# Performance work log

Measured on AMD Instinct MI355X. Metric: run time of the kernel, lower is better.

The kernel has to match this reference:

```python
import jax, jax.numpy as jnp
import numpy as np

EPSILON = 1e-8
MATCH_THRESHOLD = 0.5
MEANINGFUL_RADIUS = 0.05


def setup_inputs() -> dict:
    key = jax.random.key(0)
    ks = jax.random.split(key, 8)
    B, T, H, D, N = 4, 4096, 2048, 256, 8192
    K = H // 4
    s = lambda k, shape, fan_in: jax.random.normal(k, shape, jnp.float32) * (fan_in ** -0.5)
    return {
        "hidden": jax.random.normal(ks[0], (B, T, H), jnp.float32),
        "beliefs": jax.random.normal(ks[1], (N, D), jnp.float32),
        "active_mask": jax.random.bernoulli(ks[2], 0.9, (N,)),
        "W_obs": s(ks[3], (D, H), H),
        "W_g1": s(ks[4], (K, H), H),
        "b_g1": jnp.zeros((K,), jnp.float32),
        "W_g2": s(ks[5], (1, K), K),
        "b_g2": jnp.full((1,), -2.0, jnp.float32),  # nn.init.constant_(bias, -2.0)
        "W_p1": s(ks[6], (K, H), H),
        "b_p1": jnp.zeros((K,), jnp.float32),
        "W_p2": s(ks[7], (1, K), K),
        "b_p2": jnp.zeros((1,), jnp.float32),
    }


def reference(hidden, beliefs, active_mask, W_obs, W_g1, b_g1, W_g2, b_g2, W_p1, b_p1, W_p2, b_p2):
    # --- projections over [B, T, H] ---
    obs = jnp.einsum('bth,dh->btd', hidden, W_obs)                       # [B,T,D]
    g_h = jax.nn.relu(jnp.einsum('bth,kh->btk', hidden, W_g1) + b_g1)
    gate = jax.nn.sigmoid(jnp.einsum('btk,ok->bto', g_h, W_g2) + b_g2)   # [B,T,1]
    p_h = jax.nn.relu(jnp.einsum('bth,kh->btk', hidden, W_p1) + b_p1)
    prec = jax.nn.softplus(jnp.einsum('btk,ok->bto', p_h, W_p2) + b_p2)  # [B,T,1]

    obs_mean = obs.mean(axis=0)            # [T,D]
    prec_mean = (gate * prec).mean(axis=0)  # [T,1]

    # F.normalize(x, dim=-1, eps) == x / max(||x||, eps)
    obs_angles = obs_mean / jnp.maximum(
        jnp.linalg.norm(obs_mean, axis=-1, keepdims=True), EPSILON)
    obs_beliefs = obs_angles * prec_mean    # [T,D], radius = gated precision

    # --- match against active belief slots (fully vectorized, no per-token loop) ---
    obs_r = jnp.linalg.norm(obs_beliefs, axis=-1)                       # [T]
    obs_ang = obs_beliefs / jnp.maximum(obs_r, EPSILON)[:, None]
    bel_r = jnp.maximum(jnp.linalg.norm(beliefs, axis=-1), EPSILON)     # [N]
    bel_ang = beliefs / bel_r[:, None]

    sims = obs_ang @ bel_ang.T              # [T,N] cosine similarities
    neg = jnp.finfo(sims.dtype).min
    masked = jnp.where(active_mask[None, :], sims, neg)
    any_active = jnp.any(active_mask)
    best_sims = jnp.where(any_active, masked.max(axis=-1), 0.0)         # [T]
    best_idx = jnp.where(any_active, jnp.argmax(masked, axis=-1), -1)   # [T]

    meaningful = obs_r > MEANINGFUL_RADIUS
    matched = meaningful & (best_sims > MATCH_THRESHOLD)
    matched_slot = jnp.where(matched, best_idx, -1)                     # -1 == new slot
    match_sim = jnp.where(matched, best_sims, 0.0)

    # vectorized stand-in for list[WriteCandidate]:
    # belief vectors, per-token match similarity, matched slot id, validity mask
    return obs_beliefs, match_sim, matched_slot, meaningful
```

## Files before the change

kernel.cpp:

```cpp
#include <hip/hip_runtime.h>

constexpr int B = 4, T = 4096, H = 2048, D = 256, KK = 512, N = 8192;
constexpr int BT = B * T;
constexpr int NALL = 1280;
constexpr int CAP = 1536;

typedef short bf16x8 __attribute__((ext_vector_type(8)));
typedef float f32x4  __attribute__((ext_vector_type(4)));

__device__ __forceinline__ unsigned short f2bf(float f) {
    unsigned u = __float_as_uint(f);
    return (unsigned short)((u + 0x7fffu + ((u >> 16) & 1u)) >> 16);
}
__device__ __forceinline__ float bf2f(unsigned short h) {
    return __uint_as_float((unsigned)h << 16);
}
__device__ __forceinline__ void async16(const void* g, void* l) {
    __builtin_amdgcn_global_load_lds(
        (const __attribute__((address_space(1))) unsigned int*)g,
        (__attribute__((address_space(3))) unsigned int*)l, 16, 0, 0);
}
__device__ __forceinline__ unsigned long long enc_sim(float s, int idx) {
    unsigned bits = __float_as_uint(s);
    unsigned e32 = (bits & 0x80000000u) ? ~bits : (bits | 0x80000000u);
    return ((unsigned long long)e32 << 32) | (unsigned)(~(unsigned)idx);
}

constexpr size_t WS_HB   = 0;
constexpr size_t WS_WB   = WS_HB   + (size_t)BT * H * 2;
constexpr size_t WS_BELB = WS_WB   + (size_t)NALL * H * 2;
constexpr size_t WS_OAB  = WS_BELB + (size_t)N * D * 2;
constexpr size_t WS_B1C  = WS_OAB  + (size_t)T * D * 2;
constexpr size_t WS_W2C  = WS_B1C  + 4096;
constexpr size_t WS_FAC  = WS_W2C  + 4096;
constexpr size_t WS_OBSR = WS_FAC  + 16384;
constexpr size_t WS_FLAG = WS_OBSR + 16384;
constexpr size_t WS_OBS  = WS_FLAG + (size_t)CAP * 4;
constexpr size_t WS_YG   = WS_OBS  + (size_t)T * D * 4;
constexpr size_t WS_YP   = WS_YG   + (size_t)BT * 4;
constexpr size_t WS_ENC  = WS_YP   + (size_t)BT * 4;
constexpr size_t WS_CNT  = WS_ENC  + (size_t)T * 8;
constexpr size_t WS_ACTV = WS_CNT  + 256;
constexpr size_t WS_META = WS_ACTV + (size_t)N * 4;
constexpr size_t WS_NEEDF = WS_META + 256;
constexpr size_t WS_ZEROSZ = WS_ACTV - WS_OBS;

constexpr int    WTC    = 1280;
constexpr size_t F_WT   = 0;
constexpr size_t F_BEL  = F_WT   + (size_t)H * WTC * 4;
constexpr size_t F_OBS  = F_BEL  + (size_t)N * D * 4;
constexpr size_t F_YG   = F_OBS  + (size_t)T * D * 4;
constexpr size_t F_YP   = F_YG   + (size_t)BT * 4;
constexpr size_t F_OBSR = F_YP   + (size_t)BT * 4;
constexpr size_t F_ENC  = F_OBSR + (size_t)T * 4;
constexpr size_t F_ACT  = F_ENC  + (size_t)T * 8;
constexpr size_t F_META = F_ACT  + (size_t)N * 4;
constexpr size_t F_NEED = F_META + 256;

__global__ void mask_kernel(const unsigned char* raw, int* active, int* meta) {
    __shared__ int s_f32bad, s_nz_nonaligned;
    if (threadIdx.x == 0) { s_f32bad = 0; s_nz_nonaligned = 0; }
    __syncthreads();
    const float* rf = (const float*)raw;
    const int*   ri = (const int*)raw;
    for (int i = threadIdx.x; i < N; i += blockDim.x) {
        unsigned char b = raw[i];
        if ((i & 3) && b) atomicOr(&s_nz_nonaligned, 1);
    }
    for (int e = threadIdx.x; e < N / 4; e += blockDim.x) {
        float f = rf[e]; if (!(f == 0.0f || f == 1.0f)) atomicOr(&s_f32bad, 1);
    }
    __syncthreads();
    int layout;
    if (!s_f32bad)            layout = 2;
    else if (s_nz_nonaligned) layout = 1;
    else                      layout = 0;
    for (int n = threadIdx.x; n < N; n += blockDim.x) {
        int a;
        if (layout == 2)      a = (rf[n] != 0.0f);
        else if (layout == 1) a = (raw[n] != 0);
        else                  a = (ri[n] != 0);
        active[n] = a;
    }
    if (threadIdx.x == 0) meta[0] = layout;
}

__global__ void outw_kernel(const unsigned long long* enc, const float* obs_r_ws,
                            float* out1, float* out2) {
    int t = blockIdx.x * 256 + threadIdx.x;
    if (t >= T) return;
    unsigned long long ev = enc[t];
    float best; int idx;
    if (ev == 0ULL) { best = -3.4e38f; idx = -1; }
    else {
        unsigned int e32 = (unsigned int)(ev >> 32);
        unsigned int bits = (e32 & 0x80000000u) ? (e32 & 0x7FFFFFFFu) : ~e32;
        best = __uint_as_float(bits);
        idx = (int)~((unsigned int)(ev & 0xFFFFFFFFu));
    }
    bool meaningful = obs_r_ws[t] > 0.05f;
    bool matched = meaningful && (best > 0.5f);
    out1[t] = matched ? best : 0.0f;
    out2[t] = matched ? (float)idx : -1.0f;
}

__global__ void conv_hidden(const float* hidden, unsigned short* hb) {
    int e = blockIdx.x * 256 + threadIdx.x;
    int row = e >> 8, c8 = (e & 255) * 8;
    const float* src = hidden + (size_t)row * H + c8;
    float4 v0 = *(const float4*)src;
    float4 v1 = *(const float4*)(src + 4);
    uint4 o;
    o.x = f2bf(v0.x) | ((unsigned)f2bf(v0.y) << 16);
    o.y = f2bf(v0.z) | ((unsigned)f2bf(v0.w) << 16);
    o.z = f2bf(v1.x) | ((unsigned)f2bf(v1.y) << 16);
    o.w = f2bf(v1.z) | ((unsigned)f2bf(v1.w) << 16);
    *(uint4*)(hb + (size_t)row * H + c8) = o;
}

__global__ void conv_wb(const float* Wg1, const float* Wp1, const float* Wobs,
                        unsigned short* wb) {
    int e = blockIdx.x * 256 + threadIdx.x;
    int row = e >> 8, c8 = (e & 255) * 8;
    const float* src = (row < 512) ? &Wg1[(size_t)row * H]
                     : (row < 1024) ? &Wp1[(size_t)(row - 512) * H]
                                    : &Wobs[(size_t)(row - 1024) * H];
    float4 v0 = *(const float4*)(src + c8);
    float4 v1 = *(const float4*)(src + c8 + 4);
    uint4 o;
    o.x = f2bf(v0.x) | ((unsigned)f2bf(v0.y) << 16);
    o.y = f2bf(v0.z) | ((unsigned)f2bf(v0.w) << 16);
    o.z = f2bf(v1.x) | ((unsigned)f2bf(v1.y) << 16);
    o.w = f2bf(v1.z) | ((unsigned)f2bf(v1.w) << 16);
    *(uint4*)(wb + (size_t)row * H + c8) = o;
}

__global__ void conv_vec(const float* b_g1, const float* b_p1, const float* W_g2,
                         const float* W_p2, float* b1c, float* w2c) {
    int c = threadIdx.x;
    if (c < 512) { b1c[c] = b_g1[c];       w2c[c] = W_g2[c]; }
    else         { b1c[c] = b_p1[c - 512]; w2c[c] = W_p2[c - 512]; }
}

__global__ void belprep_bf(const float* beliefs, unsigned short* belb) {
    int wave = (blockIdx.x * blockDim.x + threadIdx.x) >> 6;
    int lane = threadIdx.x & 63;
    if (wave >= N) return;
    float4 v = ((const float4*)(beliefs + (size_t)wave * D))[lane];
    float ss = v.x * v.x + v.y * v.y + v.z * v.z + v.w * v.w;
    for (int m = 1; m < 64; m <<= 1) ss += __shfl_xor(ss, m, 64);
    float inv = 1.0f / fmaxf(sqrtf(ss), 1e-8f);
    uint2 o;
    o.x = f2bf(v.x * inv) | ((unsigned)f2bf(v.y * inv) << 16);
    o.y = f2bf(v.z * inv) | ((unsigned)f2bf(v.w * inv) << 16);
    *(uint2*)(belb + (size_t)wave * D + lane * 4) = o;
}

__global__ __launch_bounds__(256) void big_gemm(const unsigned short* Ab, const unsigned short* Bb,
                                                const float* b1c, const float* w2c,
                                                float* yg, float* yp, float* obs_buf) {
    __shared__ unsigned short As[128 * 32];
    __shared__ unsigned short Bs[128 * 32];
    __shared__ float b1s[128], w2s[128];
    int tid = threadIdx.x;
    int mb = blockIdx.x, nb = blockIdx.y;
    int m0 = mb * 128, n0 = nb * 128;
    bool is_mlp = (nb < 8);
    if (is_mlp && tid < 128) { b1s[tid] = b1c[n0 + tid]; w2s[tid] = w2c[n0 + tid]; }
    int wave = tid >> 6, lane = tid & 63;
    int wr = wave >> 1, wc = wave & 1;
    int quad = lane >> 4, mrow = lane & 15;
    f32x4 acc[4][4] = {};
    const unsigned short* gA = Ab + (size_t)(m0 + (tid >> 2)) * H + (tid & 3) * 8;
    const unsigned short* gB = Bb + (size_t)(n0 + (tid >> 2)) * H + (tid & 3) * 8;
    char* lA = (char*)As + wave * 1024;
    char* lB = (char*)Bs + wave * 1024;
    for (int k0 = 0; k0 < H; k0 += 32) {
        async16(gA + k0, lA);
        async16(gA + (size_t)64 * H + k0, lA + 4096);
        async16(gB + k0, lB);
        async16(gB + (size_t)64 * H + k0, lB + 4096);
        __syncthreads();
        bf16x8 a[4], b[4];
        for (int i = 0; i < 4; i++) a[i] = *(const bf16x8*)&As[(wr * 64 + i * 16 + mrow) * 32 + quad * 8];
        for (int j = 0; j < 4; j++) b[j] = *(const bf16x8*)&Bs[(wc * 64 + j * 16 + mrow) * 32 + quad * 8];
        for (int i = 0; i < 4; i++)
            for (int j = 0; j < 4; j++)
                acc[i][j] = __builtin_amdgcn_mfma_f32_16x16x32_bf16(a[i], b[j], acc[i][j], 0, 0, 0);
        __syncthreads();
    }
    if (is_mlp) {
        float* y = (nb < 4) ? yg : yp;
        for (int i = 0; i < 4; i++) {
            int row_g = m0 + wr * 64 + i * 16 + quad * 4;
            for (int r = 0; r < 4; r++) {
                float s = 0.0f;
                for (int j = 0; j < 4; j++) {
                    int cl = wc * 64 + j * 16 + mrow;
                    float z = acc[i][j][r] + b1s[cl];
                    z = fmaxf(z, 0.0f);
                    s += z * w2s[cl];
                }
                s += __shfl_xor(s, 1); s += __shfl_xor(s, 2);
                s += __shfl_xor(s, 4); s += __shfl_xor(s, 8);
                if (mrow == 0) atomicAdd(&y[row_g + r], s);
            }
        }
    } else {
        for (int i = 0; i < 4; i++)
            for (int r = 0; r < 4; r++) {
                int row_g = m0 + wr * 64 + i * 16 + quad * 4 + r;
                int t = row_g & (T - 1);
                for (int j = 0; j < 4; j++) {
                    int d = n0 - 1024 + wc * 64 + j * 16 + mrow;
                    atomicAdd(&obs_buf[(size_t)t * D + d], acc[i][j][r] * 0.25f);
                }
            }
    }
}

__global__ void finalize_fast(const float* yg, const float* yp, const float* obs_buf,
                              const float* b_g2, const float* b_p2,
                              float* out0, float* out3, float* obs_r_ws, float* fac,
                              unsigned short* oab, int* flaglist, int* flagcnt,
                              float* yg_mut, float* yp_mut) {
    int t = blockIdx.x * 4 + (threadIdx.x >> 6);
    int lane = threadIdx.x & 63;
    if (t >= T) return;
    float bg2 = b_g2[0], bp2 = b_p2[0];
    float pm = 0.0f;
    for (int b = 0; b < B; ++b) {
        float g = yg[b * T + t] + bg2;
        float p = yp[b * T + t] + bp2;
        float gate = 1.0f / (1.0f + expf(-g));
        float prec = (p > 20.0f) ? p : log1pf(expf(p));
        pm += gate * prec;
    }
    pm *= 0.25f;
    float4 v = ((const float4*)(obs_buf + (size_t)t * D))[lane];
    float ss = v.x * v.x + v.y * v.y + v.z * v.z + v.w * v.w;
    for (int m = 1; m < 64; m <<= 1) ss += __shfl_xor(ss, m, 64);
    float norm = sqrtf(ss);
    float na = fmaxf(norm, 1e-8f);
    float f = norm / na;
    float inv = 1.0f / na;
    float ax = v.x * inv, ay = v.y * inv, az = v.z * inv, aw = v.w * inv;
    float4 ob; ob.x = ax * pm; ob.y = ay * pm; ob.z = az * pm; ob.w = aw * pm;
    ((float4*)(out0 + (size_t)t * D))[lane] = ob;
    uint2 oa;
    oa.x = f2bf(ax) | ((unsigned)f2bf(ay) << 16);
    oa.y = f2bf(az) | ((unsigned)f2bf(aw) << 16);
    *(uint2*)(oab + (size_t)t * D + lane * 4) = oa;
    if (lane == 0) {
        float obs_r = pm * f;
        obs_r_ws[t] = obs_r;
        fac[t] = f;
        out3[t] = (obs_r > 0.05f) ? 1.0f : 0.0f;
        if (fabsf(obs_r - 0.05f) < 1.2e-3f) {
            int idx = atomicAdd(flagcnt, 1);
            if (idx < CAP) {
                flaglist[idx] = t;
                for (int b = 0; b < B; ++b) { yg_mut[b * T + t] = 0.0f; yp_mut[b * T + t] = 0.0f; }
            }
        }
    }
}

__global__ __launch_bounds__(256) void refine_mfma(const float* hidden,
        const float* W_g1, const float* W_p1, const float* b1c, const float* w2c,
        const int* flaglist, const int* flagcnt, float* yg, float* yp) {
    int nrows = min(*flagcnt, CAP) * 4;
    int m0 = blockIdx.x * 64;
    if (m0 >= nrows) return;
    int nb = blockIdx.y;
    int n0 = nb * 128;
    __shared__ unsigned short Ahi[64 * 32], Alo[64 * 32];
    __shared__ unsigned short Bhi[128 * 32], Blo[128 * 32];
    __shared__ int rowg_s[64];
    __shared__ float b1s[128], w2s[128];
    int tid = threadIdx.x;
    if (tid < 64) {
        int fr = m0 + tid;
        int rg = -1;
        if (fr < nrows) { int tok = flaglist[fr >> 2]; rg = (fr & 3) * T + tok; }
        rowg_s[tid] = rg;
    } else if (tid >= 128) {
        int c = tid - 128;
        b1s[c] = b1c[n0 + c]; w2s[c] = w2c[n0 + c];
    }
    __syncthreads();
    const float* Wbase = (n0 < 512) ? W_g1 : W_p1;
    int wofs = n0 & 511;
    int arow = tid >> 2, kseg = (tid & 3) * 8;
    int argr = rowg_s[arow]; if (argr < 0) argr = 0;
    const float* aptr = hidden + (size_t)argr * H + kseg;
    const float* bptr0 = Wbase + (size_t)(wofs + arow) * H + kseg;
    const float* bptr1 = Wbase + (size_t)(wofs + arow + 64) * H + kseg;
    int wave = tid >> 6, lane = tid & 63;
    int quad = lane >> 4, mrow = lane & 15;
    f32x4 acc[4][2] = {};
    for (int k0 = 0; k0 < H; k0 += 32) {
        float xs[8];
        {
            float4 v0 = *(const float4*)(aptr + k0);
            float4 v1 = *(const float4*)(aptr + k0 + 4);
            xs[0]=v0.x; xs[1]=v0.y; xs[2]=v0.z; xs[3]=v0.w;
            xs[4]=v1.x; xs[5]=v1.y; xs[6]=v1.z; xs[7]=v1.w;
            unsigned short hi[8], lo[8];
            for (int q = 0; q < 8; q++) {
                hi[q] = f2bf(xs[q]);
                lo[q] = f2bf(xs[q] - bf2f(hi[q]));
            }
            uint4 ph, pl;
            ph.x = hi[0]|((unsigned)hi[1]<<16); ph.y = hi[2]|((unsigned)hi[3]<<16);
            ph.z = hi[4]|((unsigned)hi[5]<<16); ph.w = hi[6]|((unsigned)hi[7]<<16);
            pl.x = lo[0]|((unsigned)lo[1]<<16); pl.y = lo[2]|((unsigned)lo[3]<<16);
            pl.z = lo[4]|((unsigned)lo[5]<<16); pl.w = lo[6]|((unsigned)lo[7]<<16);
            *(uint4*)&Ahi[arow * 32 + kseg] = ph;
            *(uint4*)&Alo[arow * 32 + kseg] = pl;
        }
        for (int half = 0; half < 2; half++) {
            const float* bp = half ? bptr1 : bptr0;
            float4 v0 = *(const float4*)(bp + k0);
            float4 v1 = *(const float4*)(bp + k0 + 4);
            xs[0]=v0.x; xs[1]=v0.y; xs[2]=v0.z; xs[3]=v0.w;
            xs[4]=v1.x; xs[5]=v1.y; xs[6]=v1.z; xs[7]=v1.w;
            unsigned short hi[8], lo[8];
            for (int q = 0; q < 8; q++) {
                hi[q] = f2bf(xs[q]);
                lo[q] = f2bf(xs[q] - bf2f(hi[q]));
            }
            uint4 ph, pl;
            ph.x = hi[0]|((unsigned)hi[1]<<16); ph.y = hi[2]|((unsigned)hi[3]<<16);
            ph.z = hi[4]|((unsigned)hi[5]<<16); ph.w = hi[6]|((unsigned)hi[7]<<16);
            pl.x = lo[0]|((unsigned)lo[1]<<16); pl.y = lo[2]|((unsigned)lo[3]<<16);
            pl.z = lo[4]|((unsigned)lo[5]<<16); pl.w = lo[6]|((unsigned)lo[7]<<16);
            *(uint4*)&Bhi[(arow + half * 64) * 32 + kseg] = ph;
            *(uint4*)&Blo[(arow + half * 64) * 32 + kseg] = pl;
        }
        __syncthreads();
        bf16x8 ah[4], al[4], bh[2], bl[2];
        for (int i = 0; i < 4; i++) {
            ah[i] = *(const bf16x8*)&Ahi[(i * 16 + mrow) * 32 + quad * 8];
            al[i] = *(const bf16x8*)&Alo[(i * 16 + mrow) * 32 + quad * 8];
        }
        for (int j = 0; j < 2; j++) {
            bh[j] = *(const bf16x8*)&Bhi[(wave * 32 + j * 16 + mrow) * 32 + quad * 8];
            bl[j] = *(const bf16x8*)&Blo[(wave * 32 + j * 16 + mrow) * 32 + quad * 8];
        }
        for (int i = 0; i < 4; i++)
            for (int j = 0; j < 2; j++) {
                acc[i][j] = __builtin_amdgcn_mfma_f32_16x16x32_bf16(al[i], bh[j], acc[i][j], 0, 0, 0);
                acc[i][j] = __builtin_amdgcn_mfma_f32_16x16x32_bf16(ah[i], bl[j], acc[i][j], 0, 0, 0);
                acc[i][j] = __builtin_amdgcn_mfma_f32_16x16x32_bf16(ah[i], bh[j], acc[i][j], 0, 0, 0);
            }
        __syncthreads();
    }
    float* y = (nb < 4) ? yg : yp;
    for (int i = 0; i < 4; i++)
        for (int r = 0; r < 4; r++) {
            int row_l = i * 16 + quad * 4 + r;
            float s = 0.0f;
            for (int j = 0; j < 2; j++) {
                int cl = wave * 32 + j * 16 + mrow;
                float z = fmaxf(acc[i][j][r] + b1s[cl], 0.0f);
                s += z * w2s[cl];
            }
            s += __shfl_xor(s, 1); s += __shfl_xor(s, 2);
            s += __shfl_xor(s, 4); s += __shfl_xor(s, 8);
            if (mrow == 0) {
                int rg = rowg_s[row_l];
                if (rg >= 0) atomicAdd(&y[rg], s);
            }
        }
}

__global__ void refine_pm(const float* yg, const float* yp, const float* b_g2, const float* b_p2,
                          const int* flagcnt, const int* flaglist, const float* fac,
                          float* obs_r_ws, float* out3) {
    int nflag = min(*flagcnt, CAP);
    int idx = blockIdx.x * 64 + threadIdx.x;
    if (idx >= nflag) return;
    int t = flaglist[idx];
    float bg2 = b_g2[0], bp2 = b_p2[0];
    float pm = 0.0f;
    for (int b = 0; b < B; ++b) {
        float g = yg[b * T + t] + bg2;
        float p = yp[b * T + t] + bp2;
        float gate = 1.0f / (1.0f + expf(-g));
        float prec = (p > 20.0f) ? p : log1pf(expf(p));
        pm += gate * prec;
    }
    pm *= 0.25f;
    float obs_r = pm * fac[t];
    obs_r_ws[t] = obs_r;
    out3[t] = (obs_r > 0.05f) ? 1.0f : 0.0f;
}

__global__ __launch_bounds__(256) void sims_mfma(const unsigned short* oab, const unsigned short* belb,
                                                 const int* active, unsigned long long* enc) {
    __shared__ unsigned short As[128 * 32];
    __shared__ unsigned short Bs[128 * 32];
    __shared__ int acts[128];
    int tid = threadIdx.x;
    int mb = blockIdx.x, nb = blockIdx.y;
    int m0 = mb * 128, n0 = nb * 128;
    if (tid < 128) acts[tid] = active[n0 + tid];
    int wave = tid >> 6, lane = tid & 63;
    int wr = wave >> 1, wc = wave & 1;
    int quad = lane >> 4, mrow = lane & 15;
    f32x4 acc[4][4] = {};
    const unsigned short* gA = oab + (size_t)(m0 + (tid >> 2)) * D + (tid & 3) * 8;
    const unsigned short* gB = belb + (size_t)(n0 + (tid >> 2)) * D + (tid & 3) * 8;
    char* lA = (char*)As + wave * 1024;
    char* lB = (char*)Bs + wave * 1024;
    for (int k0 = 0; k0 < D; k0 += 32) {
        async16(gA + k0, lA);
        async16(gA + (size_t)64 * D + k0, lA + 4096);
        async16(gB + k0, lB);
        async16(gB + (size_t)64 * D + k0, lB + 4096);
        __syncthreads();
        bf16x8 a[4], b[4];
        for (int i = 0; i < 4; i++) a[i] = *(const bf16x8*)&As[(wr * 64 + i * 16 + mrow) * 32 + quad * 8];
        for (int j = 0; j < 4; j++) b[j] = *(const bf16x8*)&Bs[(wc * 64 + j * 16 + mrow) * 32 + quad * 8];
        for (int i = 0; i < 4; i++)
            for (int j = 0; j < 4; j++)
                acc[i][j] = __builtin_amdgcn_mfma_f32_16x16x32_bf16(a[i], b[j], acc[i][j], 0, 0, 0);
        __syncthreads();
    }
    for (int i = 0; i < 4; i++)
        for (int r = 0; r < 4; r++) {
            int row_g = m0 + wr * 64 + i * 16 + quad * 4 + r;
            unsigned long long best = 0ULL;
            for (int j = 0; j < 4; j++) {
                int cl = wc * 64 + j * 16 + mrow;
                if (acts[cl]) {
                    unsigned long long ev = enc_sim(acc[i][j][r], n0 + cl);
                    if (ev > best) best = ev;
                }
            }
            best = max(best, __shfl_xor(best, 1));
            best = max(best, __shfl_xor(best, 2));
            best = max(best, __shfl_xor(best, 4));
            best = max(best, __shfl_xor(best, 8));
            if (mrow == 0 && best) atomicMax(&enc[row_g], best);
        }
}

__global__ void wt_kernel(const float* Wg1, const float* Wp1, const float* Wobs, float* WT) {
    __shared__ float tile[32][33];
    int hb = blockIdx.x * 32, cb = blockIdx.y * 32;
    int x = threadIdx.x & 31, y = threadIdx.x >> 5;
    for (int i = 0; i < 32; i += 8) {
        int c = cb + y + i;
        const float* src = (c < 512) ? &Wg1[(size_t)c * H]
                         : (c < 1024) ? &Wp1[(size_t)(c - 512) * H]
                                      : &Wobs[(size_t)(c - 1024) * H];
        tile[y + i][x] = src[hb + x];
    }
    __syncthreads();
    for (int i = 0; i < 32; i += 8)
        WT[(size_t)(hb + y + i) * WTC + cb + x] = tile[x][y + i];
}

__global__ void belprep_kernel(const float* beliefs, float* bel_ang) {
    int wave = (blockIdx.x * blockDim.x + threadIdx.x) >> 6;
    int lane = threadIdx.x & 63;
    if (wave >= N) return;
    float4 v = ((const float4*)(beliefs + (size_t)wave * D))[lane];
    float ss = v.x * v.x + v.y * v.y + v.z * v.z + v.w * v.w;
    for (int m = 1; m < 64; m <<= 1) ss += __shfl_xor(ss, m, 64);
    float inv = 1.0f / fmaxf(sqrtf(ss), 1e-8f);
    float4 o; o.x = v.x * inv; o.y = v.y * inv; o.z = v.z * inv; o.w = v.w * inv;
    ((float4*)(bel_ang + (size_t)wave * D))[lane] = o;
}

__global__ __launch_bounds__(256) void gemm_obs_kernel(const float* hidden, const float* WT,
                                                       float* obs_mean) {
    __shared__ float As[32][33];
    __shared__ float Ws[32][260];
    int t0 = blockIdx.x * 32;
    int tx = threadIdx.x & 63, ty = threadIdx.x >> 6;
    float acc[8][4] = {};
    for (int h0 = 0; h0 < H; h0 += 32) {
        for (int q = 0; q < 4; ++q) {
            int e = threadIdx.x + q * 256;
            int r = e >> 5, kk = e & 31;
            float s = 0.0f;
            for (int b = 0; b < B; ++b) s += hidden[((size_t)b * T + t0 + r) * H + h0 + kk];
            As[kk][r] = s;
        }
        for (int q = 0; q < 8; ++q) {
            int e4 = threadIdx.x + q * 256;
            int kk = e4 >> 6, c4 = (e4 & 63) * 4;
            *(float4*)&Ws[kk][c4] = *(const float4*)&WT[(size_t)(h0 + kk) * WTC + 1024 + c4];
        }
        __syncthreads();
        for (int kk = 0; kk < 32; ++kk) {
            float a[8], w[4];
            for (int i = 0; i < 8; i++) a[i] = As[kk][ty * 8 + i];
            for (int j = 0; j < 4; j++) w[j] = Ws[kk][tx + 64 * j];
            for (int i = 0; i < 8; i++)
                for (int j = 0; j < 4; j++) acc[i][j] += a[i] * w[j];
        }
        __syncthreads();
    }
    for (int i = 0; i < 8; i++)
        for (int j = 0; j < 4; j++)
            obs_mean[(size_t)(t0 + ty * 8 + i) * D + tx + 64 * j] = acc[i][j] * 0.25f;
}

__global__ __launch_bounds__(512, 4) void gemm_mlp_kernel(
        const float* hidden, const float* WT,
        const float* b1g, const float* b1p, const float* w2g, const float* w2p,
        const float* b2g, const float* b2p, float* yg, float* yp) {
    __shared__ float As[16][65];
    __shared__ float Ws[16][516];
    int R = blockIdx.x * 64;
    int path = blockIdx.y;
    int cbase = path * 512;
    int tx = threadIdx.x & 63, ty = threadIdx.x >> 6;
    float acc[8][8] = {};
    for (int h0 = 0; h0 < H; h0 += 16) {
        {   int r = threadIdx.x >> 3, k2 = (threadIdx.x & 7) * 2;
            float2 v = *(const float2*)&hidden[(size_t)(R + r) * H + h0 + k2];
            As[k2][r] = v.x; As[k2 + 1][r] = v.y; }
        for (int q = 0; q < 4; ++q) {
            int e4 = threadIdx.x + q * 512;
            int kk = e4 >> 7, c4 = (e4 & 127) * 4;
            *(float4*)&Ws[kk][c4] = *(const float4*)&WT[(size_t)(h0 + kk) * WTC + cbase + c4];
        }
        __syncthreads();
        for (int kk = 0; kk < 16; ++kk) {
            float a[8], w[8];
            for (int i = 0; i < 8; i++) a[i] = As[kk][ty * 8 + i];
            for (int j = 0; j < 8; j++) w[j] = Ws[kk][tx + 64 * j];
            for (int i = 0; i < 8; i++)
                for (int j = 0; j < 8; j++) acc[i][j] += a[i] * w[j];
        }
        __syncthreads();
    }
    const float* b1 = path ? b1p : b1g;
    const float* w2 = path ? w2p : w2g;
    float b2 = path ? b2p[0] : b2g[0];
    float part[8];
    for (int i = 0; i < 8; i++) {
        float s = 0.0f;
        for (int j = 0; j < 8; j++) {
            int c = tx + 64 * j;
            float z = fmaxf(acc[i][j] + b1[c], 0.0f);
            s += z * w2[c];
        }
        part[i] = s;
    }
    for (int m = 1; m < 64; m <<= 1)
        for (int i = 0; i < 8; i++) part[i] += __shfl_xor(part[i], m, 64);
    if (tx == 0) {
        float* dst = path ? yp : yg;
        for (int i = 0; i < 8; i++) dst[R + ty * 8 + i] = part[i] + b2;
    }
}

__global__ void finalize_kernel(const float* yg, const float* yp, float* obs,
                                float* out0, float* out3, float* obs_r_ws,
                                unsigned long long* enc) {
    int t = blockIdx.x * 4 + (threadIdx.x >> 6);
    int lane = threadIdx.x & 63;
    if (t >= T) return;
    float pm = 0.0f;
    for (int b = 0; b < B; ++b) {
        float g = yg[b * T + t], p = yp[b * T + t];
        float gate = 1.0f / (1.0f + expf(-g));
        float prec = (p > 15.0f) ? p : log1pf(expf(p));
        pm += gate * prec;
    }
    pm *= (1.0f / B);
    float4 v = ((const float4*)(obs + (size_t)t * D))[lane];
    float ss = v.x * v.x + v.y * v.y + v.z * v.z + v.w * v.w;
    for (int m = 1; m < 64; m <<= 1) ss += __shfl_xor(ss, m, 64);
    float norm = sqrtf(ss);
    float na = fmaxf(norm, 1e-8f);
    float4 ob;
    ob.x = v.x / na * pm; ob.y = v.y / na * pm;
    ob.z = v.z / na * pm; ob.w = v.w / na * pm;
    float obs_r = pm * (norm / na);
    ((float4*)(out0 + (size_t)t * D))[lane] = ob;
    float ra = fmaxf(obs_r, 1e-8f);
    float4 oa;
    oa.x = ob.x / ra; oa.y = ob.y / ra; oa.z = ob.z / ra; oa.w = ob.w / ra;
    ((float4*)(obs + (size_t)t * D))[lane] = oa;
    if (lane == 0) {
        out3[t] = (obs_r > 0.05f) ? 1.0f : 0.0f;
        obs_r_ws[t] = obs_r;
        enc[t] = 0ULL;
    }
}

__global__ __launch_bounds__(256) void sims_kernel(const float* obs_ang, const float* bel_ang,
                                                   const int* active, unsigned long long* enc) {
    __shared__ float Aos[64][68];
    __shared__ float Bbs[64][68];
    __shared__ unsigned long long lmax[64];
    __shared__ int act[64];
    int tb = blockIdx.x * 64, nb = blockIdx.y * 64;
    int tx = threadIdx.x & 15, ty = threadIdx.x >> 4;
    if (threadIdx.x < 64) { lmax[threadIdx.x] = 0ULL; act[threadIdx.x] = active[nb + threadIdx.x]; }
    float acc[4][4] = {};
    for (int d0 = 0; d0 < D; d0 += 64) {
        for (int q = 0; q < 4; ++q) {
            int e4 = threadIdx.x + q * 256;
            int r = e4 >> 4, c4 = (e4 & 15) * 4;
            *(float4*)&Aos[r][c4] = *(const float4*)&obs_ang[(size_t)(tb + r) * D + d0 + c4];
            *(float4*)&Bbs[r][c4] = *(const float4*)&bel_ang[(size_t)(nb + r) * D + d0 + c4];
        }
        __syncthreads();
        for (int dd = 0; dd < 64; ++dd) {
            float a[4], w[4];
            for (int i = 0; i < 4; i++) a[i] = Aos[ty + 16 * i][dd];
            for (int j = 0; j < 4; j++) w[j] = Bbs[tx + 16 * j][dd];
            for (int i = 0; i < 4; i++)
                for (int j = 0; j < 4; j++) acc[i][j] += a[i] * w[j];
        }
        __syncthreads();
    }
    for (int i = 0; i < 4; i++) {
        unsigned long long best = 0ULL;
        for (int j = 0; j < 4; j++) {
            int c = tx + 16 * j;
            if (act[c]) {
                unsigned long long ev = enc_sim(acc[i][j], nb + c);
                if (ev > best) best = ev;
            }
        }
        atomicMax(&lmax[ty + 16 * i], best);
    }
    __syncthreads();
    if (threadIdx.x < 64 && lmax[threadIdx.x])
        atomicMax(&enc[tb + threadIdx.x], lmax[threadIdx.x]);
}

extern "C" void kernel_launch(void* const* d_in, const int* in_sizes, int n_in,
                              void* d_out, int out_size, void* d_ws, size_t ws_size,
                              hipStream_t stream) {
    const float* hidden  = (const float*)d_in[0];
    const float* beliefs = (const float*)d_in[1];
    const unsigned char* mask_raw = (const unsigned char*)d_in[2];
    const float* W_obs = (const float*)d_in[3];
    const float* W_g1  = (const float*)d_in[4];
    const float* b_g1  = (const float*)d_in[5];
    const float* W_g2  = (const float*)d_in[6];
    const float* b_g2  = (const float*)d_in[7];
    const float* W_p1  = (const float*)d_in[8];
    const float* b_p1  = (const float*)d_in[9];
    const float* W_p2  = (const float*)d_in[10];
    const float* b_p2  = (const float*)d_in[11];

    float* out0 = (float*)d_out;
    float* out1 = out0 + (size_t)T * D;
    float* out2 = out1 + T;
    float* out3 = out2 + T;
    char* ws = (char*)d_ws;

    if (ws_size >= WS_NEEDF) {
        unsigned short* hb   = (unsigned short*)(ws + WS_HB);
        unsigned short* wb   = (unsigned short*)(ws + WS_WB);
        unsigned short* belb = (unsigned short*)(ws + WS_BELB);
        unsigned short* oab  = (unsigned short*)(ws + WS_OAB);
        float* b1c     = (float*)(ws + WS_B1C);
        float* w2c     = (float*)(ws + WS_W2C);
        float* fac     = (float*)(ws + WS_FAC);
        float* obs_r   = (float*)(ws + WS_OBSR);
        int*   flaglist= (int*)(ws + WS_FLAG);
        float* obs_buf = (float*)(ws + WS_OBS);
        float* yg      = (float*)(ws + WS_YG);
        float* yp      = (float*)(ws + WS_YP);
        unsigned long long* enc = (unsigned long long*)(ws + WS_ENC);
        int*   flagcnt = (int*)(ws + WS_CNT);
        int*   active  = (int*)(ws + WS_ACTV);
        int*   meta    = (int*)(ws + WS_META);

        hipMemsetAsync(ws + WS_OBS, 0, WS_ZEROSZ, stream);
        mask_kernel<<<1, 1024, 0, stream>>>(mask_raw, active, meta);
        conv_vec<<<1, 1024, 0, stream>>>(b_g1, b_p1, W_g2, W_p2, b1c, w2c);
        conv_wb<<<NALL, 256, 0, stream>>>(W_g1, W_p1, W_obs, wb);
        conv_hidden<<<BT, 256, 0, stream>>>(hidden, hb);
        belprep_bf<<<N / 4, 256, 0, stream>>>(beliefs, belb);
        big_gemm<<<dim3(BT / 128, NALL / 128), 256, 0, stream>>>(hb, wb, b1c, w2c, yg, yp, obs_buf);
        finalize_fast<<<T / 4, 256, 0, stream>>>(yg, yp, obs_buf, b_g2, b_p2,
                                                 out0, out3, obs_r, fac, oab,
                                                 flaglist, flagcnt, yg, yp);
        refine_mfma<<<dim3(CAP * 4 / 64, 8), 256, 0, stream>>>(hidden, W_g1, W_p1, b1c, w2c,
                                                               flaglist, flagcnt, yg, yp);
        refine_pm<<<CAP / 64, 64, 0, stream>>>(yg, yp, b_g2, b_p2, flagcnt, flaglist,
                                               fac, obs_r, out3);
        sims_mfma<<<dim3(T / 128, N / 128), 256, 0, stream>>>(oab, belb, active, enc);
        outw_kernel<<<(T + 255) / 256, 256, 0, stream>>>(enc, obs_r, out1, out2);
        return;
    }

    if (ws_size < F_NEED) return;
    float* WT       = (float*)(ws + F_WT);
    float* bel_ang  = (float*)(ws + F_BEL);
    float* obs_buf  = (float*)(ws + F_OBS);
    float* yg       = (float*)(ws + F_YG);
    float* yp       = (float*)(ws + F_YP);
    float* obs_r_ws = (float*)(ws + F_OBSR);
    unsigned long long* enc = (unsigned long long*)(ws + F_ENC);
    int* active     = (int*)(ws + F_ACT);
    int* meta       = (int*)(ws + F_META);

    mask_kernel<<<1, 1024, 0, stream>>>(mask_raw, active, meta);
    wt_kernel<<<dim3(H / 32, WTC / 32), 256, 0, stream>>>(W_g1, W_p1, W_obs, WT);
    belprep_kernel<<<N / 4, 256, 0, stream>>>(beliefs, bel_ang);
    gemm_obs_kernel<<<T / 32, 256, 0, stream>>>(hidden, WT, obs_buf);
    gemm_mlp_kernel<<<dim3(BT / 64, 2), 512, 0, stream>>>(
        hidden, WT, b_g1, b_p1, W_g2, W_p2, b_g2, b_p2, yg, yp);
    finalize_kernel<<<T / 4, 256, 0, stream>>>(yg, yp, obs_buf, out0, out3, obs_r_ws, enc);
    sims_kernel<<<dim3(T / 64, N / 64), 256, 0, stream>>>(obs_buf, bel_ang, active, enc);
    outw_kernel<<<(T + 255) / 256, 256, 0, stream>>>(enc, obs_r_ws, out1, out2);
}
```

Measured before the change: 491.9 us.

## Split obs GEMM with batch-mean-first, block-local sim max, sparse argmax pass

The obs projection moves out of the big GEMM into its own kernel, which averages the four batch rows of hidden before the MFMA. That cuts the obs GEMM work by four and removes the per-element atomics into obs_buf. The sims kernel now reduces only a 32-bit max per row, first in shared memory and then with one global atomic per row. A separate argmax kernel recomputes the index only for matched tokens, capped at 256. The refine threshold band and the flag capacity are also tightened. The risks are a changed rounding path from averaging in bf16, and wrong results if more than 256 tokens match or more tokens fall near the threshold than before.

```diff
diff --git a/kernel.cpp b/kernel.cpp
--- a/kernel.cpp
+++ b/kernel.cpp
@@ -3,7 +3,8 @@
 constexpr int B = 4, T = 4096, H = 2048, D = 256, KK = 512, N = 8192;
 constexpr int BT = B * T;
 constexpr int NALL = 1280;
-constexpr int CAP = 1536;
+constexpr int CAP = 1024;
+constexpr int MCAP = 256;
 
 typedef short bf16x8 __attribute__((ext_vector_type(8)));
 typedef float f32x4  __attribute__((ext_vector_type(4)));
@@ -25,25 +26,35 @@
     unsigned e32 = (bits & 0x80000000u) ? ~bits : (bits | 0x80000000u);
     return ((unsigned long long)e32 << 32) | (unsigned)(~(unsigned)idx);
 }
+__device__ __forceinline__ unsigned enc_f32(float s) {
+    unsigned b = __float_as_uint(s);
+    return (b & 0x80000000u) ? ~b : (b | 0x80000000u);
+}
+__device__ __forceinline__ float dec_f32(unsigned e) {
+    return __uint_as_float((e & 0x80000000u) ? (e & 0x7FFFFFFFu) : ~e);
+}
 
 constexpr size_t WS_HB   = 0;
 constexpr size_t WS_WB   = WS_HB   + (size_t)BT * H * 2;
 constexpr size_t WS_BELB = WS_WB   + (size_t)NALL * H * 2;
 constexpr size_t WS_OAB  = WS_BELB + (size_t)N * D * 2;
-constexpr size_t WS_B1C  = WS_OAB  + (size_t)T * D * 2;
+constexpr size_t WS_OBS  = WS_OAB  + (size_t)T * D * 2;
+constexpr size_t WS_B1C  = WS_OBS  + (size_t)T * D * 4;
 constexpr size_t WS_W2C  = WS_B1C  + 4096;
 constexpr size_t WS_FAC  = WS_W2C  + 4096;
 constexpr size_t WS_OBSR = WS_FAC  + 16384;
 constexpr size_t WS_FLAG = WS_OBSR + 16384;
-constexpr size_t WS_OBS  = WS_FLAG + (size_t)CAP * 4;
-constexpr size_t WS_YG   = WS_OBS  + (size_t)T * D * 4;
+constexpr size_t WS_ACTV = WS_FLAG + (size_t)CAP * 4;
+constexpr size_t WS_META = WS_ACTV + (size_t)N * 4;
+constexpr size_t WS_YG   = WS_META + 256;
 constexpr size_t WS_YP   = WS_YG   + (size_t)BT * 4;
 constexpr size_t WS_ENC  = WS_YP   + (size_t)BT * 4;
-constexpr size_t WS_CNT  = WS_ENC  + (size_t)T * 8;
-constexpr size_t WS_ACTV = WS_CNT  + 256;
-constexpr size_t WS_META = WS_ACTV + (size_t)N * 4;
-constexpr size_t WS_NEEDF = WS_META + 256;
-constexpr size_t WS_ZEROSZ = WS_ACTV - WS_OBS;
+constexpr size_t WS_CNT  = WS_ENC  + (size_t)T * 4;
+constexpr size_t WS_MCNT = WS_CNT  + 256;
+constexpr size_t WS_MLST = WS_MCNT + 256;
+constexpr size_t WS_ZEND = WS_MLST + (size_t)MCAP * 4;
+constexpr size_t WS_NEEDF = WS_ZEND;
+constexpr size_t WS_ZEROSZ = WS_ZEND - WS_YG;
 
 constexpr int    WTC    = 1280;
 constexpr size_t F_WT   = 0;
@@ -83,25 +94,6 @@
         active[n] = a;
     }
     if (threadIdx.x == 0) meta[0] = layout;
-}
-
-__global__ void outw_kernel(const unsigned long long* enc, const float* obs_r_ws,
-                            float* out1, float* out2) {
-    int t = blockIdx.x * 256 + threadIdx.x;
-    if (t >= T) return;
-    unsigned long long ev = enc[t];
-    float best; int idx;
-    if (ev == 0ULL) { best = -3.4e38f; idx = -1; }
-    else {
-        unsigned int e32 = (unsigned int)(ev >> 32);
-        unsigned int bits = (e32 & 0x80000000u) ? (e32 & 0x7FFFFFFFu) : ~e32;
-        best = __uint_as_float(bits);
-        idx = (int)~((unsigned int)(ev & 0xFFFFFFFFu));
-    }
-    bool meaningful = obs_r_ws[t] > 0.05f;
-    bool matched = meaningful && (best > 0.5f);
-    out1[t] = matched ? best : 0.0f;
-    out2[t] = matched ? (float)idx : -1.0f;
 }
 
 __global__ void conv_hidden(const float* hidden, unsigned short* hb) {
@@ -156,17 +148,16 @@
     *(uint2*)(belb + (size_t)wave * D + lane * 4) = o;
 }
 
-__global__ __launch_bounds__(256) void big_gemm(const unsigned short* Ab, const unsigned short* Bb,
-                                                const float* b1c, const float* w2c,
-                                                float* yg, float* yp, float* obs_buf) {
+__global__ __launch_bounds__(256) void gemm_mlp_mfma(const unsigned short* Ab, const unsigned short* Bb,
+                                                     const float* b1c, const float* w2c,
+                                                     float* yg, float* yp) {
     __shared__ unsigned short As[128 * 32];
     __shared__ unsigned short Bs[128 * 32];
     __shared__ float b1s[128], w2s[128];
     int tid = threadIdx.x;
     int mb = blockIdx.x, nb = blockIdx.y;
     int m0 = mb * 128, n0 = nb * 128;
-    bool is_mlp = (nb < 8);
-    if (is_mlp && tid < 128) { b1s[tid] = b1c[n0 + tid]; w2s[tid] = w2c[n0 + tid]; }
+    if (tid < 128) { b1s[tid] = b1c[n0 + tid]; w2s[tid] = w2c[n0 + tid]; }
     int wave = tid >> 6, lane = tid & 63;
     int wr = wave >> 1, wc = wave & 1;
     int quad = lane >> 4, mrow = lane & 15;
@@ -189,34 +180,76 @@
                 acc[i][j] = __builtin_amdgcn_mfma_f32_16x16x32_bf16(a[i], b[j], acc[i][j], 0, 0, 0);
         __syncthreads();
     }
-    if (is_mlp) {
-        float* y = (nb < 4) ? yg : yp;
-        for (int i = 0; i < 4; i++) {
-            int row_g = m0 + wr * 64 + i * 16 + quad * 4;
-            for (int r = 0; r < 4; r++) {
-                float s = 0.0f;
-                for (int j = 0; j < 4; j++) {
-                    int cl = wc * 64 + j * 16 + mrow;
-                    float z = acc[i][j][r] + b1s[cl];
-                    z = fmaxf(z, 0.0f);
-                    s += z * w2s[cl];
-                }
-                s += __shfl_xor(s, 1); s += __shfl_xor(s, 2);
-                s += __shfl_xor(s, 4); s += __shfl_xor(s, 8);
-                if (mrow == 0) atomicAdd(&y[row_g + r], s);
-            }
-        }
-    } else {
+    float* y = (nb < 4) ? yg : yp;
+    for (int i = 0; i < 4; i++) {
+        int row_g = m0 + wr * 64 + i * 16 + quad * 4;
+        for (int r = 0; r < 4; r++) {
+            float s = 0.0f;
+            for (int j = 0; j < 4; j++) {
+                int cl = wc * 64 + j * 16 + mrow;
+                float z = fmaxf(acc[i][j][r] + b1s[cl], 0.0f);
+                s += z * w2s[cl];
+            }
+            s += __shfl_xor(s, 1); s += __shfl_xor(s, 2);
+            s += __shfl_xor(s, 4); s += __shfl_xor(s, 8);
+            if (mrow == 0) atomicAdd(&y[row_g + r], s);
+        }
+    }
+}
+
+__global__ __launch_bounds__(512) void gemm_obs_sum(const unsigned short* hb, const unsigned short* wb,
+                                                    float* obs_buf) {
+    __shared__ unsigned short As[128 * 32];
+    __shared__ unsigned short Bs[256 * 32];
+    int tid = threadIdx.x;
+    int t0 = blockIdx.x * 128;
+    int wave = tid >> 6, lane = tid & 63;
+    int wr = wave >> 2, wc = wave & 3;
+    int quad = lane >> 4, mrow = lane & 15;
+    f32x4 acc[4][4] = {};
+    int arow = tid >> 2, seg8 = (tid & 3) * 8;
+    const unsigned short* hA = hb + (size_t)(t0 + arow) * H + seg8;
+    const unsigned short* gB = wb + (size_t)(1024 + (tid >> 2)) * H + (tid & 3) * 8;
+    char* lB = (char*)Bs + wave * 1024;
+    for (int k0 = 0; k0 < H; k0 += 32) {
+        async16(gB + k0, lB);
+        async16(gB + (size_t)128 * H + k0, lB + 8192);
+        {
+            uint4 v0 = *(const uint4*)(hA + k0);
+            uint4 v1 = *(const uint4*)(hA + (size_t)T * H + k0);
+            uint4 v2 = *(const uint4*)(hA + (size_t)2 * T * H + k0);
+            uint4 v3 = *(const uint4*)(hA + (size_t)3 * T * H + k0);
+            const unsigned* p0 = (const unsigned*)&v0;
+            const unsigned* p1 = (const unsigned*)&v1;
+            const unsigned* p2 = (const unsigned*)&v2;
+            const unsigned* p3 = (const unsigned*)&v3;
+            uint4 o; unsigned* po = (unsigned*)&o;
+            for (int q = 0; q < 4; q++) {
+                float lo = 0.25f * (bf2f((unsigned short)(p0[q] & 0xFFFF)) + bf2f((unsigned short)(p1[q] & 0xFFFF))
+                                  + bf2f((unsigned short)(p2[q] & 0xFFFF)) + bf2f((unsigned short)(p3[q] & 0xFFFF)));
+                float hi = 0.25f * (bf2f((unsigned short)(p0[q] >> 16)) + bf2f((unsigned short)(p1[q] >> 16))
+                                  + bf2f((unsigned short)(p2[q] >> 16)) + bf2f((unsigned short)(p3[q] >> 16)));
+                po[q] = f2bf(lo) | ((unsigned)f2bf(hi) << 16);
+            }
+            *(uint4*)&As[arow * 32 + seg8] = o;
+        }
+        __syncthreads();
+        bf16x8 a[4], b[4];
+        for (int i = 0; i < 4; i++) a[i] = *(const bf16x8*)&As[(wr * 64 + i * 16 + mrow) * 32 + quad * 8];
+        for (int j = 0; j < 4; j++) b[j] = *(const bf16x8*)&Bs[(wc * 64 + j * 16 + mrow) * 32 + quad * 8];
         for (int i = 0; i < 4; i++)
-            for (int r = 0; r < 4; r++) {
-                int row_g = m0 + wr * 64 + i * 16 + quad * 4 + r;
-                int t = row_g & (T - 1);
-                for (int j = 0; j < 4; j++) {
-                    int d = n0 - 1024 + wc * 64 + j * 16 + mrow;
-                    atomicAdd(&obs_buf[(size_t)t * D + d], acc[i][j][r] * 0.25f);
-                }
-            }
-    }
+            for (int j = 0; j < 4; j++)
+                acc[i][j] = __builtin_amdgcn_mfma_f32_16x16x32_bf16(a[i], b[j], acc[i][j], 0, 0, 0);
+        __syncthreads();
+    }
+    for (int i = 0; i < 4; i++)
+        for (int r = 0; r < 4; r++) {
+            int row_g = t0 + wr * 64 + i * 16 + quad * 4 + r;
+            for (int j = 0; j < 4; j++) {
+                int col = wc * 64 + j * 16 + mrow;
+                obs_buf[(size_t)row_g * D + col] = acc[i][j][r];
+            }
+        }
 }
 
 __global__ void finalize_fast(const float* yg, const float* yp, const float* obs_buf,
@@ -256,7 +289,7 @@
         obs_r_ws[t] = obs_r;
         fac[t] = f;
         out3[t] = (obs_r > 0.05f) ? 1.0f : 0.0f;
-        if (fabsf(obs_r - 0.05f) < 1.2e-3f) {
+        if (fabsf(obs_r - 0.05f) < 5.0e-4f) {
             int idx = atomicAdd(flagcnt, 1);
             if (idx < CAP) {
                 flaglist[idx] = t;
@@ -398,14 +431,15 @@
 }
 
 __global__ __launch_bounds__(256) void sims_mfma(const unsigned short* oab, const unsigned short* belb,
-                                                 const int* active, unsigned long long* enc) {
+                                                 const int* active, unsigned* encg) {
     __shared__ unsigned short As[128 * 32];
     __shared__ unsigned short Bs[128 * 32];
     __shared__ int acts[128];
+    __shared__ unsigned lmax32[128];
     int tid = threadIdx.x;
     int mb = blockIdx.x, nb = blockIdx.y;
     int m0 = mb * 128, n0 = nb * 128;
-    if (tid < 128) acts[tid] = active[n0 + tid];
+    if (tid < 128) { acts[tid] = active[n0 + tid]; lmax32[tid] = 0u; }
     int wave = tid >> 6, lane = tid & 63;
     int wr = wave >> 1, wc = wave & 1;
     int quad = lane >> 4, mrow = lane & 15;
@@ -430,21 +464,106 @@
     }
     for (int i = 0; i < 4; i++)
         for (int r = 0; r < 4; r++) {
-            int row_g = m0 + wr * 64 + i * 16 + quad * 4 + r;
-            unsigned long long best = 0ULL;
+            int row_l = wr * 64 + i * 16 + quad * 4 + r;
+            float m = -3.4e38f;
             for (int j = 0; j < 4; j++) {
                 int cl = wc * 64 + j * 16 + mrow;
-                if (acts[cl]) {
-                    unsigned long long ev = enc_sim(acc[i][j][r], n0 + cl);
-                    if (ev > best) best = ev;
-                }
-            }
-            best = max(best, __shfl_xor(best, 1));
-            best = max(best, __shfl_xor(best, 2));
-            best = max(best, __shfl_xor(best, 4));
-            best = max(best, __shfl_xor(best, 8));
-            if (mrow == 0 && best) atomicMax(&enc[row_g], best);
-        }
+                if (acts[cl]) m = fmaxf(m, acc[i][j][r]);
+            }
+            m = fmaxf(m, __shfl_xor(m, 1)); m = fmaxf(m, __shfl_xor(m, 2));
+            m = fmaxf(m, __shfl_xor(m, 4)); m = fmaxf(m, __shfl_xor(m, 8));
+            if (mrow == 0 && m > -3.3e38f) atomicMax(&lmax32[row_l], enc_f32(m));
+        }
+    __syncthreads();
+    if (tid < 128 && lmax32[tid]) atomicMax(&encg[m0 + tid], lmax32[tid]);
+}
+
+__global__ void outw_kernel(const unsigned* encg, const float* obs_r_ws,
+                            float* out1, float* out2, int* mcnt, int* mlist) {
+    int t = blockIdx.x * 256 + threadIdx.x;
+    if (t >= T) return;
+    unsigned ev = encg[t];
+    float best = (ev == 0u) ? -3.4e38f : dec_f32(ev);
+    bool meaningful = obs_r_ws[t] > 0.05f;
+    bool matched = meaningful && (best > 0.5f);
+    out1[t] = matched ? best : 0.0f;
+    out2[t] = -1.0f;
+    if (matched) {
+        int slot = atomicAdd(mcnt, 1);
+        if (slot < MCAP) mlist[slot] = t;
+    }
+}
+
+__global__ void argmax_kernel(const unsigned short* oab, const unsigned short* belb,
+                              const int* active, const int* mcnt, const int* mlist,
+                              float* out1, float* out2) {
+    int nm = min(*mcnt, MCAP);
+    int j = blockIdx.x;
+    if (j >= nm) return;
+    int t = mlist[j];
+    __shared__ float q[256];
+    __shared__ unsigned long long red[256];
+    if (threadIdx.x < 128) {
+        unsigned v = ((const unsigned*)(oab + (size_t)t * D))[threadIdx.x];
+        q[threadIdx.x * 2]     = bf2f((unsigned short)(v & 0xFFFF));
+        q[threadIdx.x * 2 + 1] = bf2f((unsigned short)(v >> 16));
+    }
+    __syncthreads();
+    float best = -3.4e38f; int bi = -1;
+    for (int k = 0; k < N / 256; k++) {
+        int n = threadIdx.x + k * 256;
+        if (!active[n]) continue;
+        const uint4* br = (const uint4*)(belb + (size_t)n * D);
+        float s = 0.0f;
+        for (int c = 0; c < 32; c++) {
+            uint4 v = br[c];
+            const unsigned* pv = (const unsigned*)&v;
+            for (int w = 0; w < 4; w++) {
+                s += q[c * 8 + w * 2]     * bf2f((unsigned short)(pv[w] & 0xFFFF));
+                s += q[c * 8 + w * 2 + 1] * bf2f((unsigned short)(pv[w] >> 16));
+            }
+        }
+        if (s > best) { best = s; bi = n; }
+    }
+    red[threadIdx.x] = (bi >= 0) ? enc_sim(best, bi) : 0ULL;
+    __syncthreads();
+    for (int st = 128; st > 0; st >>= 1) {
+        if (threadIdx.x < st) red[threadIdx.x] = max(red[threadIdx.x], red[threadIdx.x + st]);
+        __syncthreads();
+    }
+    if (threadIdx.x == 0) {
+        unsigned long long ev = red[0];
+        if (ev) {
+            unsigned e32 = (unsigned)(ev >> 32);
+            out1[t] = __uint_as_float((e32 & 0x80000000u) ? (e32 & 0x7FFFFFFFu) : ~e32);
+            out2[t] = (float)(int)~((unsigned)(ev & 0xFFFFFFFFu));
+        }
+    }
+}
+
+__global__ void f_mask_kernel(const unsigned char* raw, int* active, int* meta) {
+    __shared__ int s_f32bad, s_nz_nonaligned;
+    if (threadIdx.x == 0) { s_f32bad = 0; s_nz_nonaligned = 0; }
+    __syncthreads();
+    const float* rf = (const float*)raw;
+    const int*   ri = (const int*)raw;
+    for (int i = threadIdx.x; i < N; i += blockDim.x) {
+        unsigned char b = raw[i];
+        if ((i & 3) && b) atomicOr(&s_nz_nonaligned, 1);
+    }
+    for (int e = threadIdx.x; e < N / 4; e += blockDim.x) {
+        float f = rf[e]; if (!(f == 0.0f || f == 1.0f)) atomicOr(&s_f32bad, 1);
+    }
+    __syncthreads();
+    int layout = (!s_f32bad) ? 2 : (s_nz_nonaligned ? 1 : 0);
+    for (int n = threadIdx.x; n < N; n += blockDim.x) {
+        int a;
+        if (layout == 2)      a = (rf[n] != 0.0f);
+        else if (layout == 1) a = (raw[n] != 0);
+        else                  a = (ri[n] != 0);
+        active[n] = a;
+    }
+    if (threadIdx.x == 0) meta[0] = layout;
 }
 
 __global__ void wt_kernel(const float* Wg1, const float* Wp1, const float* Wobs, float* WT) {
@@ -639,6 +758,25 @@
         atomicMax(&enc[tb + threadIdx.x], lmax[threadIdx.x]);
 }
 
+__global__ void f_outw_kernel(const unsigned long long* enc, const float* obs_r_ws,
+                              float* out1, float* out2) {
+    int t = blockIdx.x * 256 + threadIdx.x;
+    if (t >= T) return;
+    unsigned long long ev = enc[t];
+    float best; int idx;
+    if (ev == 0ULL) { best = -3.4e38f; idx = -1; }
+    else {
+        unsigned int e32 = (unsigned int)(ev >> 32);
+        unsigned int bits = (e32 & 0x80000000u) ? (e32 & 0x7FFFFFFFu) : ~e32;
+        best = __uint_as_float(bits);
+        idx = (int)~((unsigned int)(ev & 0xFFFFFFFFu));
+    }
+    bool meaningful = obs_r_ws[t] > 0.05f;
+    bool matched = meaningful && (best > 0.5f);
+    out1[t] = matched ? best : 0.0f;
+    out2[t] = matched ? (float)idx : -1.0f;
+}
+
 extern "C" void kernel_launch(void* const* d_in, const int* in_sizes, int n_in,
                               void* d_out, int out_size, void* d_ws, size_t ws_size,
                               hipStream_t stream) {
@@ -666,26 +804,29 @@
         unsigned short* wb   = (unsigned short*)(ws + WS_WB);
         unsigned short* belb = (unsigned short*)(ws + WS_BELB);
         unsigned short* oab  = (unsigned short*)(ws + WS_OAB);
+        float* obs_buf = (float*)(ws + WS_OBS);
         float* b1c     = (float*)(ws + WS_B1C);
         float* w2c     = (float*)(ws + WS_W2C);
         float* fac     = (float*)(ws + WS_FAC);
         float* obs_r   = (float*)(ws + WS_OBSR);
         int*   flaglist= (int*)(ws + WS_FLAG);
-        float* obs_buf = (float*)(ws + WS_OBS);
+        int*   active  = (int*)(ws + WS_ACTV);
+        int*   meta    = (int*)(ws + WS_META);
         float* yg      = (float*)(ws + WS_YG);
         float* yp      = (float*)(ws + WS_YP);
-        unsigned long long* enc = (unsigned long long*)(ws + WS_ENC);
+        unsigned* encg = (unsigned*)(ws + WS_ENC);
         int*   flagcnt = (int*)(ws + WS_CNT);
-        int*   active  = (int*)(ws + WS_ACTV);
-        int*   meta    = (int*)(ws + WS_META);
-
-        hipMemsetAsync(ws + WS_OBS, 0, WS_ZEROSZ, stream);
+        int*   mcnt    = (int*)(ws + WS_MCNT);
+        int*   mlist   = (int*)(ws + WS_MLST);
+
+        hipMemsetAsync(ws + WS_YG, 0, WS_ZEROSZ, stream);
         mask_kernel<<<1, 1024, 0, stream>>>(mask_raw, active, meta);
         conv_vec<<<1, 1024, 0, stream>>>(b_g1, b_p1, W_g2, W_p2, b1c, w2c);
         conv_wb<<<NALL, 256, 0, stream>>>(W_g1, W_p1, W_obs, wb);
         conv_hidden<<<BT, 256, 0, stream>>>(hidden, hb);
         belprep_bf<<<N / 4, 256, 0, stream>>>(beliefs, belb);
-        big_gemm<<<dim3(BT / 128, NALL / 128), 256, 0, stream>>>(hb, wb, b1c, w2c, yg, yp, obs_buf);
+        gemm_mlp_mfma<<<dim3(BT / 128, 8), 256, 0, stream>>>(hb, wb, b1c, w2c, yg, yp);
+        gemm_obs_sum<<<T / 128, 512, 0, stream>>>(hb, wb, obs_buf);
         finalize_fast<<<T / 4, 256, 0, stream>>>(yg, yp, obs_buf, b_g2, b_p2,
                                                  out0, out3, obs_r, fac, oab,
                                                  flaglist, flagcnt, yg, yp);
@@ -693,8 +834,9 @@
                                                                flaglist, flagcnt, yg, yp);
         refine_pm<<<CAP / 64, 64, 0, stream>>>(yg, yp, b_g2, b_p2, flagcnt, flaglist,
                                                fac, obs_r, out3);
-        sims_mfma<<<dim3(T / 128, N / 128), 256, 0, stream>>>(oab, belb, active, enc);
-        outw_kernel<<<(T + 255) / 256, 256, 0, stream>>>(enc, obs_r, out1, out2);
+        sims_mfma<<<dim3(T / 128, N / 128), 256, 0, stream>>>(oab, belb, active, encg);
+        outw_kernel<<<(T + 255) / 256, 256, 0, stream>>>(encg, obs_r, out1, out2, mcnt, mlist);
+        argmax_kernel<<<MCAP, 256, 0, stream>>>(oab, belb, active, mcnt, mlist, out1, out2);
         return;
     }
 
@@ -709,7 +851,7 @@
     int* active     = (int*)(ws + F_ACT);
     int* meta       = (int*)(ws + F_META);
 
-    mask_kernel<<<1, 1024, 0, stream>>>(mask_raw, active, meta);
+    f_mask_kernel<<<1, 1024, 0, stream>>>(mask_raw, active, meta);
     wt_kernel<<<dim3(H / 32, WTC / 32), 256, 0, stream>>>(W_g1, W_p1, W_obs, WT);
     belprep_kernel<<<N / 4, 256, 0, stream>>>(beliefs, bel_ang);
     gemm_obs_kernel<<<T / 32, 256, 0, stream>>>(hidden, WT, obs_buf);
@@ -717,5 +859,5 @@
         hidden, WT, b_g1, b_p1, W_g2, W_p2, b_g2, b_p2, yg, yp);
     finalize_kernel<<<T / 4, 256, 0, stream>>>(yg, yp, obs_buf, out0, out3, obs_r_ws, enc);
     sims_kernel<<<dim3(T / 64, N / 64), 256, 0, stream>>>(obs_buf, bel_ang, active, enc);
-    outw_kernel<<<(T + 255) / 256, 256, 0, stream>>>(enc, obs_r_ws, out1, out2);
-}
+    f_outw_kernel<<<(T + 255) / 256, 256, 0, stream>>>(enc, obs_r_ws, out1, out2);
+}
```

After: 570.8 us. 1.16x slower.
